# Optimization experiments

Hardware: AMD Instinct MI355X
Metric: run time of the kernel (lower is better)

Reference implementation:

```python
import jax, jax.numpy as jnp
import numpy as np

N, E, B = 50000, 640000, 4
H, L = 128, 4
NODE_IN, EDGE_IN, COND_IN, NODE_OUT = 12, 4, 10, 3


def _mlp(x, w1, b1, w2, b2):
    # Linear -> ReLU -> Linear
    return jnp.maximum(x @ w1 + b1, 0.0) @ w2 + b2


def setup_inputs() -> dict:
    key = jax.random.key(0)
    keys = iter(jax.random.split(key, 64))

    def p(*shape):
        fan_in = shape[-2] if len(shape) >= 2 else shape[-1]
        return (jax.random.normal(next(keys), shape, jnp.float32) / np.sqrt(fan_in)).astype(jnp.float32)

    inp = {
        "x": jax.random.normal(next(keys), (N, NODE_IN), jnp.float32),
        "edge_index": jax.random.randint(next(keys), (2, E), 0, N),
        "edge_attr": jax.random.normal(next(keys), (E, EDGE_IN), jnp.float32),
        "conditions": jax.random.normal(next(keys), (B, COND_IN), jnp.float32),
        "batch": jnp.sort(jax.random.randint(next(keys), (N,), 0, B)),
        # encoders
        "enc_node_w1": p(NODE_IN, H), "enc_node_b1": jnp.zeros((H,), jnp.float32),
        "enc_node_w2": p(H, H), "enc_node_b2": jnp.zeros((H,), jnp.float32),
        "enc_edge_w1": p(EDGE_IN, H), "enc_edge_b1": jnp.zeros((H,), jnp.float32),
        "enc_edge_w2": p(H, H), "enc_edge_b2": jnp.zeros((H,), jnp.float32),
        "enc_cond_w1": p(COND_IN, H), "enc_cond_b1": jnp.zeros((H,), jnp.float32),
        "enc_cond_w2": p(H, H), "enc_cond_b2": jnp.zeros((H,), jnp.float32),
        # shared MultiheadAttention: with a single key, softmax weight == 1 per head,
        # so output = out_proj(v_proj(kv)); q/k projections cancel exactly (and have
        # identically zero gradient), so only v/out projections are materialized.
        "attn_wv": p(H, H), "attn_bv": jnp.zeros((H,), jnp.float32),
        "attn_wo": p(H, H), "attn_bo": jnp.zeros((H,), jnp.float32),
        # processor layers (stacked over L)
        "pe_w1": p(L, 4 * H, H), "pe_b1": jnp.zeros((L, H), jnp.float32),
        "pe_w2": p(L, H, H), "pe_b2": jnp.zeros((L, H), jnp.float32),
        "pn_w1": p(L, 3 * H, H), "pn_b1": jnp.zeros((L, H), jnp.float32),
        "pn_w2": p(L, H, H), "pn_b2": jnp.zeros((L, H), jnp.float32),
        # decoder
        "dec_w1": p(H, H), "dec_b1": jnp.zeros((H,), jnp.float32),
        "dec_w2": p(H, NODE_OUT), "dec_b2": jnp.zeros((NODE_OUT,), jnp.float32),
    }
    return inp


def reference(x, edge_index, edge_attr, conditions, batch,
              enc_node_w1, enc_node_b1, enc_node_w2, enc_node_b2,
              enc_edge_w1, enc_edge_b1, enc_edge_w2, enc_edge_b2,
              enc_cond_w1, enc_cond_b1, enc_cond_w2, enc_cond_b2,
              attn_wv, attn_bv, attn_wo, attn_bo,
              pe_w1, pe_b1, pe_w2, pe_b2,
              pn_w1, pn_b1, pn_w2, pn_b2,
              dec_w1, dec_b1, dec_w2, dec_b2):
    n = x.shape[0]
    h = _mlp(x, enc_node_w1, enc_node_b1, enc_node_w2, enc_node_b2)           # [N,H]
    e = _mlp(edge_attr, enc_edge_w1, enc_edge_b1, enc_edge_w2, enc_edge_b2)   # [E,H]
    u = _mlp(conditions, enc_cond_w1, enc_cond_b1, enc_cond_w2, enc_cond_b2)  # [B,H]

    row, col = edge_index[0], edge_index[1]
    u_nodes = u[batch]                                                        # [N,H]
    # single-key cross-attention -> softmax over 1 key == 1 -> out_proj(v_proj(u))
    x_cond = (u_nodes @ attn_wv + attn_bv) @ attn_wo + attn_bo               # [N,H], same every layer
    u_edges = u_nodes[row]                                                    # u[batch[row]]

    for l in range(pe_w1.shape[0]):
        # edge update: cat([src, dest, edge_attr, u[batch_e]]) -> MLP
        e = _mlp(jnp.concatenate([h[row], h[col], e, u_edges], axis=1),
                 pe_w1[l], pe_b1[l], pe_w2[l], pe_b2[l])
        # scatter-add aggregation (index_add on row)
        agg = jax.ops.segment_sum(e, row, num_segments=n)                     # [N,H]
        # node update with residual
        h = h + _mlp(jnp.concatenate([h, agg, x_cond], axis=1),
                     pn_w1[l], pn_b1[l], pn_w2[l], pn_b2[l])

    return _mlp(h, dec_w1, dec_b1, dec_w2, dec_b2)                            # [N,node_out]
```

## Files before the change

kernel.cpp:

```cpp
#include <hip/hip_runtime.h>
#include <cstddef>

#define NN 50000
#define NNP 50048
#define NE 640000
#define NB 4
#define H  128
#define NL 4
#define TE 64
#define TEE 128

typedef unsigned int u32;
typedef unsigned short u16;
typedef __attribute__((ext_vector_type(8))) short bf16x8;
typedef __attribute__((ext_vector_type(4))) float f32x4;

__device__ __forceinline__ float bf2f(u16 s) {
    union { u32 u; float f; } v; v.u = ((u32)s) << 16; return v.f;
}
__device__ __forceinline__ u16 f2bf(float f) {
    union { float f; u32 u; } v; v.f = f;
    u32 u = v.u;
    u += 0x7FFF + ((u >> 16) & 1);
    return (u16)(u >> 16);
}
__device__ __forceinline__ void unpack8(uint4 raw, float* d) {
    d[0] = bf2f(raw.x & 0xFFFF); d[1] = bf2f(raw.x >> 16);
    d[2] = bf2f(raw.y & 0xFFFF); d[3] = bf2f(raw.y >> 16);
    d[4] = bf2f(raw.z & 0xFFFF); d[5] = bf2f(raw.z >> 16);
    d[6] = bf2f(raw.w & 0xFFFF); d[7] = bf2f(raw.w >> 16);
}
__device__ __forceinline__ uint4 pack8(const float* s) {
    uint4 pk;
    pk.x = (u32)f2bf(s[0]) | ((u32)f2bf(s[1]) << 16);
    pk.y = (u32)f2bf(s[2]) | ((u32)f2bf(s[3]) << 16);
    pk.z = (u32)f2bf(s[4]) | ((u32)f2bf(s[5]) << 16);
    pk.w = (u32)f2bf(s[6]) | ((u32)f2bf(s[7]) << 16);
    return pk;
}
__device__ __forceinline__ bf16x8 ld_f32_bf8(const float* __restrict__ p) {
    const float4 a = *(const float4*)p;
    const float4 b = *(const float4*)(p + 4);
    bf16x8 r;
    r[0] = (short)f2bf(a.x); r[1] = (short)f2bf(a.y);
    r[2] = (short)f2bf(a.z); r[3] = (short)f2bf(a.w);
    r[4] = (short)f2bf(b.x); r[5] = (short)f2bf(b.y);
    r[6] = (short)f2bf(b.z); r[7] = (short)f2bf(b.w);
    return r;
}

__global__ __launch_bounds__(256) void k_zero(float* __restrict__ p, int n4) {
    const int i = blockIdx.x * 256 + threadIdx.x;
    if (i < n4) ((float4*)p)[i] = make_float4(0.f, 0.f, 0.f, 0.f);
}

__global__ __launch_bounds__(256) void k_hist(const int* __restrict__ rowi,
                                              u32* __restrict__ cnt) {
    const int i = blockIdx.x * 256 + threadIdx.x;
    if (i < NE) atomicAdd(&cnt[rowi[i]], 1u);
}

__global__ __launch_bounds__(1024) void k_scan(u32* __restrict__ cnt) {
    __shared__ u32 part[1024];
    const int t = threadIdx.x;
    const int CHUNK = (NN + 1023) / 1024;
    const int lo = t * CHUNK;
    const int hi = (lo + CHUNK < NN) ? lo + CHUNK : NN;
    u32 s = 0;
    for (int i = lo; i < hi; ++i) s += cnt[i];
    part[t] = s;
    __syncthreads();
    for (int ofs = 1; ofs < 1024; ofs <<= 1) {
        const u32 v = (t >= ofs) ? part[t - ofs] : 0u;
        __syncthreads();
        part[t] += v;
        __syncthreads();
    }
    u32 run = (t == 0) ? 0u : part[t - 1];
    for (int i = lo; i < hi; ++i) { const u32 c = cnt[i]; cnt[i] = run; run += c; }
}

__global__ __launch_bounds__(256) void k_scatter(const int* __restrict__ rowi,
                                                 const int* __restrict__ coli,
                                                 u32* __restrict__ off,
                                                 int* __restrict__ permS,
                                                 int* __restrict__ rowS,
                                                 int* __restrict__ colS) {
    const int i = blockIdx.x * 256 + threadIdx.x;
    if (i < NE) {
        const int r = rowi[i];
        const u32 p = atomicAdd(&off[r], 1u);
        permS[p] = i; rowS[p] = r; colS[p] = coli[i];
    }
}

__global__ __launch_bounds__(256) void k_prep(
    const float* __restrict__ pe_w1, const float* __restrict__ pe_w2,
    const float* __restrict__ pn_w1, const float* __restrict__ pn_w2,
    const float* __restrict__ ew2,   const float* __restrict__ nw2,
    const float* __restrict__ dw1,
    u16* __restrict__ W1t, u16* __restrict__ W2t,
    u16* __restrict__ WaT, u16* __restrict__ WbT,
    u16* __restrict__ Wn1aT, u16* __restrict__ Wn1bT, u16* __restrict__ Wn2T,
    u16* __restrict__ W2et, u16* __restrict__ W2nt, u16* __restrict__ W1dt) {
    const int li = blockIdx.x;
    const float* src; u16* dst;
    switch (blockIdx.y) {
        case 0: src = pe_w1 + ((size_t)li * 512 + 256) * H; dst = W1t  + (size_t)li * H * H; break;
        case 1: src = pe_w2 + (size_t)li * H * H;           dst = W2t  + (size_t)li * H * H; break;
        case 2: src = pe_w1 + (size_t)li * 512 * H;         dst = WaT  + (size_t)li * H * H; break;
        case 3: src = pe_w1 + ((size_t)li * 512 + 128) * H; dst = WbT  + (size_t)li * H * H; break;
        case 4: src = pn_w1 + (size_t)li * 384 * H;         dst = Wn1aT + (size_t)li * H * H; break;
        case 5: src = pn_w1 + ((size_t)li * 384 + 128) * H; dst = Wn1bT + (size_t)li * H * H; break;
        case 6: src = pn_w2 + (size_t)li * H * H;           dst = Wn2T + (size_t)li * H * H; break;
        default:
            if (li == 0)      { src = ew2; dst = W2et; }
            else if (li == 1) { src = nw2; dst = W2nt; }
            else if (li == 2) { src = dw1; dst = W1dt; }
            else return;
            break;
    }
    for (int idx = threadIdx.x; idx < H * H; idx += 256) {
        const int n = idx >> 7, k = idx & 127;
        dst[idx] = f2bf(src[(size_t)k * H + n]);
    }
}

__global__ __launch_bounds__(128) void k_small(
    const float* __restrict__ cond,
    const float* __restrict__ ecw1, const float* __restrict__ ecb1,
    const float* __restrict__ ecw2, const float* __restrict__ ecb2,
    const float* __restrict__ wv, const float* __restrict__ bv,
    const float* __restrict__ wo, const float* __restrict__ bo,
    const float* __restrict__ pe_w1, const float* __restrict__ pe_b1,
    const float* __restrict__ pn_w1, const float* __restrict__ pn_b1,
    float* __restrict__ cbat, float* __restrict__ nbat) {
    __shared__ float tmp[NB][H];
    __shared__ float uL[NB][H];
    __shared__ float xcL[NB][H];
    const int t = threadIdx.x;
    for (int b = 0; b < NB; ++b) {
        float a = ecb1[t];
        for (int k = 0; k < 10; ++k) a = fmaf(cond[b * 10 + k], ecw1[k * H + t], a);
        tmp[b][t] = fmaxf(a, 0.f);
    }
    __syncthreads();
    for (int b = 0; b < NB; ++b) {
        float a = ecb2[t];
        for (int k = 0; k < H; ++k) a = fmaf(tmp[b][k], ecw2[k * H + t], a);
        uL[b][t] = a;
    }
    __syncthreads();
    for (int b = 0; b < NB; ++b) {
        float a = bv[t];
        for (int k = 0; k < H; ++k) a = fmaf(uL[b][k], wv[k * H + t], a);
        tmp[b][t] = a;
    }
    __syncthreads();
    for (int b = 0; b < NB; ++b) {
        float a = bo[t];
        for (int k = 0; k < H; ++k) a = fmaf(tmp[b][k], wo[k * H + t], a);
        xcL[b][t] = a;
    }
    __syncthreads();
    for (int l = 0; l < NL; ++l) {
        const float* w1u = pe_w1 + ((size_t)l * 512 + 384) * H;
        for (int b = 0; b < NB; ++b) {
            float a = pe_b1[l * H + t];
            for (int k = 0; k < H; ++k) a = fmaf(uL[b][k], w1u[k * H + t], a);
            cbat[(l * NB + b) * H + t] = a;
        }
        const float* w1x = pn_w1 + ((size_t)l * 384 + 256) * H;
        for (int b = 0; b < NB; ++b) {
            float a = pn_b1[l * H + t];
            for (int k = 0; k < H; ++k) a = fmaf(xcL[b][k], w1x[k * H + t], a);
            nbat[(l * NB + b) * H + t] = a;
        }
    }
}

__global__ __launch_bounds__(256) void k_enc_e_mfma(
    const float* __restrict__ ea,
    const int* __restrict__ permS,
    const float* __restrict__ w1, const float* __restrict__ b1,
    const u16* __restrict__ W2et, const float* __restrict__ b2,
    u16* __restrict__ e) {
    __shared__ float SI[TE][H + 4];
    const int t = threadIdx.x;
    const long long e0 = (long long)blockIdx.x * TE;
    const int w = t >> 6, l = t & 63;
    const int m16 = l & 15, g = l >> 4;
    const int row = w * 16 + m16;

    const int src = permS[e0 + row];
    const float4 av = *(const float4*)&ea[(size_t)src * 4];

    bf16x8 afrag[4];
#pragma unroll
    for (int ks = 0; ks < 4; ++ks) {
        const int c0 = ks * 32 + g * 8;
        float hv[8];
        {
            const float4 ba = *(const float4*)&b1[c0];
            const float4 bb = *(const float4*)&b1[c0 + 4];
            hv[0] = ba.x; hv[1] = ba.y; hv[2] = ba.z; hv[3] = ba.w;
            hv[4] = bb.x; hv[5] = bb.y; hv[6] = bb.z; hv[7] = bb.w;
        }
#pragma unroll
        for (int k = 0; k < 4; ++k) {
            const float s = (k == 0) ? av.x : (k == 1) ? av.y : (k == 2) ? av.z : av.w;
            const float4 wa = *(const float4*)&w1[k * H + c0];
            const float4 wb = *(const float4*)&w1[k * H + c0 + 4];
            hv[0] = fmaf(s, wa.x, hv[0]); hv[1] = fmaf(s, wa.y, hv[1]);
            hv[2] = fmaf(s, wa.z, hv[2]); hv[3] = fmaf(s, wa.w, hv[3]);
            hv[4] = fmaf(s, wb.x, hv[4]); hv[5] = fmaf(s, wb.y, hv[5]);
            hv[6] = fmaf(s, wb.z, hv[6]); hv[7] = fmaf(s, wb.w, hv[7]);
        }
#pragma unroll
        for (int j = 0; j < 8; ++j) afrag[ks][j] = (short)f2bf(fmaxf(hv[j], 0.f));
    }

    f32x4 acc[8];
#pragma unroll
    for (int nt = 0; nt < 8; ++nt) {
        const float bb = b2[nt * 16 + m16];
        acc[nt][0] = bb; acc[nt][1] = bb; acc[nt][2] = bb; acc[nt][3] = bb;
    }
#pragma unroll
    for (int ks = 0; ks < 4; ++ks) {
#pragma unroll
        for (int nt = 0; nt < 8; ++nt) {
            const bf16x8 bfr =
                *(const bf16x8*)&W2et[(size_t)(nt * 16 + m16) * H + ks * 32 + g * 8];
            acc[nt] = __builtin_amdgcn_mfma_f32_16x16x32_bf16(afrag[ks], bfr, acc[nt], 0, 0, 0);
        }
    }

#pragma unroll
    for (int nt = 0; nt < 8; ++nt)
#pragma unroll
        for (int j = 0; j < 4; ++j)
            SI[w * 16 + g * 4 + j][nt * 16 + m16] = acc[nt][j];
    __syncthreads();
    for (int u = t; u < TE * 16; u += 256) {
        const int j = u >> 4, c8 = (u & 15) * 8;
        *(uint4*)&e[(size_t)(e0 + j) * H + c8] = pack8(&SI[j][c8]);
    }
}

__global__ __launch_bounds__(256) void k_enc_n_mfma(
    const float* __restrict__ x,
    const float* __restrict__ w1, const float* __restrict__ b1,
    const u16* __restrict__ W2nt, const float* __restrict__ b2,
    float* __restrict__ h) {
    __shared__ float SI[TE][H + 4];
    const int t = threadIdx.x;
    const long long n0 = (long long)blockIdx.x * TE;
    const int w = t >> 6, l = t & 63;
    const int m16 = l & 15, g = l >> 4;
    const int row = w * 16 + m16;
    const long long nr = (n0 + row < NN) ? (n0 + row) : (NN - 1);

    float av[12];
    {
        const float4 a0 = *(const float4*)&x[nr * 12];
        const float4 a1 = *(const float4*)&x[nr * 12 + 4];
        const float4 a2 = *(const float4*)&x[nr * 12 + 8];
        av[0] = a0.x; av[1] = a0.y; av[2] = a0.z; av[3] = a0.w;
        av[4] = a1.x; av[5] = a1.y; av[6] = a1.z; av[7] = a1.w;
        av[8] = a2.x; av[9] = a2.y; av[10] = a2.z; av[11] = a2.w;
    }

    bf16x8 afrag[4];
#pragma unroll
    for (int ks = 0; ks < 4; ++ks) {
        const int c0 = ks * 32 + g * 8;
        float hv[8];
        {
            const float4 ba = *(const float4*)&b1[c0];
            const float4 bb = *(const float4*)&b1[c0 + 4];
            hv[0] = ba.x; hv[1] = ba.y; hv[2] = ba.z; hv[3] = ba.w;
            hv[4] = bb.x; hv[5] = bb.y; hv[6] = bb.z; hv[7] = bb.w;
        }
#pragma unroll
        for (int k = 0; k < 12; ++k) {
            const float s = av[k];
            const float4 wa = *(const float4*)&w1[k * H + c0];
            const float4 wb = *(const float4*)&w1[k * H + c0 + 4];
            hv[0] = fmaf(s, wa.x, hv[0]); hv[1] = fmaf(s, wa.y, hv[1]);
            hv[2] = fmaf(s, wa.z, hv[2]); hv[3] = fmaf(s, wa.w, hv[3]);
            hv[4] = fmaf(s, wb.x, hv[4]); hv[5] = fmaf(s, wb.y, hv[5]);
            hv[6] = fmaf(s, wb.z, hv[6]); hv[7] = fmaf(s, wb.w, hv[7]);
        }
#pragma unroll
        for (int j = 0; j < 8; ++j) afrag[ks][j] = (short)f2bf(fmaxf(hv[j], 0.f));
    }

    f32x4 acc[8];
#pragma unroll
    for (int nt = 0; nt < 8; ++nt) {
        const float bb = b2[nt * 16 + m16];
        acc[nt][0] = bb; acc[nt][1] = bb; acc[nt][2] = bb; acc[nt][3] = bb;
    }
#pragma unroll
    for (int ks = 0; ks < 4; ++ks) {
#pragma unroll
        for (int nt = 0; nt < 8; ++nt) {
            const bf16x8 bfr =
                *(const bf16x8*)&W2nt[(size_t)(nt * 16 + m16) * H + ks * 32 + g * 8];
            acc[nt] = __builtin_amdgcn_mfma_f32_16x16x32_bf16(afrag[ks], bfr, acc[nt], 0, 0, 0);
        }
    }

#pragma unroll
    for (int nt = 0; nt < 8; ++nt)
#pragma unroll
        for (int j = 0; j < 4; ++j)
            SI[w * 16 + g * 4 + j][nt * 16 + m16] = acc[nt][j];
    __syncthreads();
    for (int u = t; u < TE * H / 4; u += 256) {
        const int j = u >> 5, c4 = (u & 31) * 4;
        *(float4*)&h[(size_t)(n0 + j) * H + c4] = *(const float4*)&SI[j][c4];
    }
}

__global__ __launch_bounds__(256) void k_gemm_dual_mfma(
    const float* __restrict__ h,
    const u16* __restrict__ WaT, const u16* __restrict__ WbT,
    const float* __restrict__ cbatl, const int* __restrict__ batch,
    u16* __restrict__ Ca, u16* __restrict__ Cb) {
    __shared__ u16 SI[TE][H + 8];
    __shared__ float CB[NB][H];
    __shared__ int bL[TE];
    const int t = threadIdx.x;
    const long long n0 = (long long)blockIdx.x * TE;
    const int w = t >> 6, l = t & 63;
    const int m16 = l & 15, g = l >> 4;
    const int row = w * 16 + m16;

    if (t < TE) {
        const long long n = n0 + t;
        bL[t] = batch[n < NN ? n : (NN - 1)];
    }
    for (int i = t; i < NB * H; i += 256) ((float*)CB)[i] = cbatl[i];

    bf16x8 afrag[4];
    {
        const float* hp = h + (size_t)(n0 + row) * H + g * 8;
#pragma unroll
        for (int ks = 0; ks < 4; ++ks) afrag[ks] = ld_f32_bf8(hp + ks * 32);
    }
    __syncthreads();

    f32x4 accA[8], accB[8];
#pragma unroll
    for (int nt = 0; nt < 8; ++nt) {
#pragma unroll
        for (int j = 0; j < 4; ++j)
            accA[nt][j] = CB[bL[w * 16 + g * 4 + j]][nt * 16 + m16];
        accB[nt][0] = 0.f; accB[nt][1] = 0.f; accB[nt][2] = 0.f; accB[nt][3] = 0.f;
    }
#pragma unroll
    for (int ks = 0; ks < 4; ++ks) {
#pragma unroll
        for (int nt = 0; nt < 8; ++nt) {
            const size_t off = (size_t)(nt * 16 + m16) * H + ks * 32 + g * 8;
            const bf16x8 ba = *(const bf16x8*)&WaT[off];
            const bf16x8 bb = *(const bf16x8*)&WbT[off];
            accA[nt] = __builtin_amdgcn_mfma_f32_16x16x32_bf16(afrag[ks], ba, accA[nt], 0, 0, 0);
            accB[nt] = __builtin_amdgcn_mfma_f32_16x16x32_bf16(afrag[ks], bb, accB[nt], 0, 0, 0);
        }
    }

#pragma unroll
    for (int s = 0; s < 2; ++s) {
        __syncthreads();
#pragma unroll
        for (int nt = 0; nt < 8; ++nt)
#pragma unroll
            for (int j = 0; j < 4; ++j)
                SI[w * 16 + g * 4 + j][nt * 16 + m16] =
                    f2bf(s ? accB[nt][j] : accA[nt][j]);
        __syncthreads();
        u16* C = s ? Cb : Ca;
        for (int u = t; u < TE * 16; u += 256) {
            const int j = u >> 4, c8 = (u & 15) * 8;
            *(uint4*)&C[(size_t)(n0 + j) * H + c8] = *(const uint4*)&SI[j][c8];
        }
    }
}

template <bool WRITE_E>
__global__ __launch_bounds__(256, 2) void k_edge_mfma(
    const u16* __restrict__ hA, const u16* __restrict__ hB,
    const u16* __restrict__ W1t, const u16* __restrict__ W2t,
    const float* __restrict__ b2,
    const int* __restrict__ rowS, const int* __restrict__ colS,
    u16* __restrict__ e, float* __restrict__ agg) {
    __shared__ u16 SI[TEE][H + 8];
    const int t = threadIdx.x;
    const long long e0 = (long long)blockIdx.x * TEE;
    const int w = t >> 6, l = t & 63;
    const int m16 = l & 15, g = l >> 4;

    bf16x8 af0[4], af1[4];
    {
        const u16* ep0 = e + (size_t)(e0 + w * 32 + m16) * H + g * 8;
        const u16* ep1 = ep0 + 16 * H;
#pragma unroll
        for (int ks = 0; ks < 4; ++ks) {
            af0[ks] = *(const bf16x8*)(ep0 + ks * 32);
            af1[ks] = *(const bf16x8*)(ep1 + ks * 32);
        }
    }

    {
        int rj[8], cj[8];
#pragma unroll
        for (int it = 0; it < 8; ++it) {
            const int j = (l + it * 64) >> 4;
            rj[it] = rowS[e0 + w * 32 + j];
            cj[it] = colS[e0 + w * 32 + j];
        }
#pragma unroll
        for (int it = 0; it < 8; ++it) {
            const int u = l + it * 64;
            const int j = u >> 4, c8 = (u & 15) * 8;
            float va[8], vb[8], sm[8];
            unpack8(*(const uint4*)&hA[(size_t)rj[it] * H + c8], va);
            unpack8(*(const uint4*)&hB[(size_t)cj[it] * H + c8], vb);
#pragma unroll
            for (int q = 0; q < 8; ++q) sm[q] = va[q] + vb[q];
            *(uint4*)&SI[w * 32 + j][c8] = pack8(sm);
        }
    }

    f32x4 acc0[8], acc1[8];
#pragma unroll
    for (int nt = 0; nt < 8; ++nt) {
#pragma unroll
        for (int j = 0; j < 4; ++j) {
            acc0[nt][j] = bf2f(SI[w * 32 + g * 4 + j][nt * 16 + m16]);
            acc1[nt][j] = bf2f(SI[w * 32 + 16 + g * 4 + j][nt * 16 + m16]);
        }
    }
#pragma unroll
    for (int ks = 0; ks < 4; ++ks) {
#pragma unroll
        for (int nt = 0; nt < 8; ++nt) {
            const bf16x8 bfr =
                *(const bf16x8*)&W1t[(size_t)(nt * 16 + m16) * H + ks * 32 + g * 8];
            acc0[nt] = __builtin_amdgcn_mfma_f32_16x16x32_bf16(af0[ks], bfr, acc0[nt], 0, 0, 0);
            acc1[nt] = __builtin_amdgcn_mfma_f32_16x16x32_bf16(af1[ks], bfr, acc1[nt], 0, 0, 0);
        }
    }

#pragma unroll
    for (int nt = 0; nt < 8; ++nt)
#pragma unroll
        for (int j = 0; j < 4; ++j) {
            SI[w * 32 + g * 4 + j][nt * 16 + m16]      = f2bf(fmaxf(acc0[nt][j], 0.f));
            SI[w * 32 + 16 + g * 4 + j][nt * 16 + m16] = f2bf(fmaxf(acc1[nt][j], 0.f));
        }

#pragma unroll
    for (int nt = 0; nt < 8; ++nt) {
        const float bb = b2[nt * 16 + m16];
        acc0[nt][0] = bb; acc0[nt][1] = bb; acc0[nt][2] = bb; acc0[nt][3] = bb;
        acc1[nt][0] = bb; acc1[nt][1] = bb; acc1[nt][2] = bb; acc1[nt][3] = bb;
    }
#pragma unroll
    for (int ks = 0; ks < 4; ++ks) {
        const bf16x8 a20 = *(const bf16x8*)&SI[w * 32 + m16][ks * 32 + g * 8];
        const bf16x8 a21 = *(const bf16x8*)&SI[w * 32 + 16 + m16][ks * 32 + g * 8];
#pragma unroll
        for (int nt = 0; nt < 8; ++nt) {
            const bf16x8 bfr =
                *(const bf16x8*)&W2t[(size_t)(nt * 16 + m16) * H + ks * 32 + g * 8];
            acc0[nt] = __builtin_amdgcn_mfma_f32_16x16x32_bf16(a20, bfr, acc0[nt], 0, 0, 0);
            acc1[nt] = __builtin_amdgcn_mfma_f32_16x16x32_bf16(a21, bfr, acc1[nt], 0, 0, 0);
        }
    }

    {
        int r[8];
#pragma unroll
        for (int j = 0; j < 4; ++j) {
            r[j]     = rowS[e0 + w * 32 + g * 4 + j];
            r[4 + j] = rowS[e0 + w * 32 + 16 + g * 4 + j];
        }
#pragma unroll
        for (int nt = 0; nt < 8; ++nt) {
            const int c = nt * 16 + m16;
            float v[8];
#pragma unroll
            for (int j = 0; j < 4; ++j) { v[j] = acc0[nt][j]; v[4 + j] = acc1[nt][j]; }
            float s = v[0];
            int prev = r[0];
#pragma unroll
            for (int j = 1; j < 8; ++j) {
                if (r[j] == prev) s += v[j];
                else { atomicAdd(&agg[(size_t)prev * H + c], s); s = v[j]; prev = r[j]; }
            }
            atomicAdd(&agg[(size_t)prev * H + c], s);
        }
    }

    if (WRITE_E) {
#pragma unroll
        for (int nt = 0; nt < 8; ++nt)
#pragma unroll
            for (int j = 0; j < 4; ++j) {
                SI[w * 32 + g * 4 + j][nt * 16 + m16]      = f2bf(acc0[nt][j]);
                SI[w * 32 + 16 + g * 4 + j][nt * 16 + m16] = f2bf(acc1[nt][j]);
            }
#pragma unroll
        for (int it = 0; it < 8; ++it) {
            const int u = l + it * 64;
            const int j = u >> 4, c8 = (u & 15) * 8;
            *(uint4*)&e[(size_t)(e0 + w * 32 + j) * H + c8] = *(const uint4*)&SI[w * 32 + j][c8];
        }
    }
}

__global__ __launch_bounds__(256) void k_node_mfma(
    const u16* __restrict__ Wn1aT, const u16* __restrict__ Wn1bT,
    const u16* __restrict__ Wn2T, const float* __restrict__ bn2,
    const float* __restrict__ nbatl, const int* __restrict__ batch,
    const float* __restrict__ agg, float* __restrict__ h) {
    __shared__ float SI[TE][H + 4];
    __shared__ float NBl[NB][H];
    __shared__ int bL[TE];
    const int t = threadIdx.x;
    const long long n0 = (long long)blockIdx.x * TE;
    if (t < TE) {
        const long long n = n0 + t;
        bL[t] = batch[n < NN ? n : (NN - 1)];
    }
    for (int i = t; i < NB * H; i += 256) ((float*)NBl)[i] = nbatl[i];

    const int w = t >> 6, l = t & 63;
    const int m16 = l & 15, g = l >> 4;
    const int row = w * 16 + m16;

    bf16x8 afrag[4];
    {
        const float* hp = h + (size_t)(n0 + row) * H + g * 8;
#pragma unroll
        for (int ks = 0; ks < 4; ++ks) afrag[ks] = ld_f32_bf8(hp + ks * 32);
    }
    __syncthreads();

    f32x4 acc[8];
#pragma unroll
    for (int nt = 0; nt < 8; ++nt)
#pragma unroll
        for (int j = 0; j < 4; ++j)
            acc[nt][j] = NBl[bL[w * 16 + g * 4 + j]][nt * 16 + m16];

#pragma unroll
    for (int ks = 0; ks < 4; ++ks)
#pragma unroll
        for (int nt = 0; nt < 8; ++nt) {
            const bf16x8 bfr =
                *(const bf16x8*)&Wn1aT[(size_t)(nt * 16 + m16) * H + ks * 32 + g * 8];
            acc[nt] = __builtin_amdgcn_mfma_f32_16x16x32_bf16(afrag[ks], bfr, acc[nt], 0, 0, 0);
        }

    {
        const float* ap = agg + (size_t)(n0 + row) * H + g * 8;
#pragma unroll
        for (int ks = 0; ks < 4; ++ks) afrag[ks] = ld_f32_bf8(ap + ks * 32);
    }
#pragma unroll
    for (int ks = 0; ks < 4; ++ks)
#pragma unroll
        for (int nt = 0; nt < 8; ++nt) {
            const bf16x8 bfr =
                *(const bf16x8*)&Wn1bT[(size_t)(nt * 16 + m16) * H + ks * 32 + g * 8];
            acc[nt] = __builtin_amdgcn_mfma_f32_16x16x32_bf16(afrag[ks], bfr, acc[nt], 0, 0, 0);
        }

#pragma unroll
    for (int nt = 0; nt < 8; ++nt)
#pragma unroll
        for (int j = 0; j < 4; ++j)
            SI[w * 16 + g * 4 + j][nt * 16 + m16] = fmaxf(acc[nt][j], 0.f);
    __syncthreads();

    f32x4 acc2[8];
#pragma unroll
    for (int nt = 0; nt < 8; ++nt) {
        const float bb = bn2[nt * 16 + m16];
        acc2[nt][0] = bb; acc2[nt][1] = bb; acc2[nt][2] = bb; acc2[nt][3] = bb;
    }
#pragma unroll
    for (int ks = 0; ks < 4; ++ks) {
        bf16x8 a2;
        const float* hp = &SI[w * 16 + m16][ks * 32 + g * 8];
#pragma unroll
        for (int j = 0; j < 8; ++j) a2[j] = (short)f2bf(hp[j]);
#pragma unroll
        for (int nt = 0; nt < 8; ++nt) {
            const bf16x8 bfr =
                *(const bf16x8*)&Wn2T[(size_t)(nt * 16 + m16) * H + ks * 32 + g * 8];
            acc2[nt] = __builtin_amdgcn_mfma_f32_16x16x32_bf16(a2, bfr, acc2[nt], 0, 0, 0);
        }
    }
    __syncthreads();

#pragma unroll
    for (int nt = 0; nt < 8; ++nt)
#pragma unroll
        for (int j = 0; j < 4; ++j)
            SI[w * 16 + g * 4 + j][nt * 16 + m16] = acc2[nt][j];
    __syncthreads();

    for (int u = t; u < TE * H / 4; u += 256) {
        const int j = u >> 5, c4 = (u & 31) * 4;
        float4 hv = *(const float4*)&h[(size_t)(n0 + j) * H + c4];
        const float4 sv = *(const float4*)&SI[j][c4];
        hv.x += sv.x; hv.y += sv.y; hv.z += sv.z; hv.w += sv.w;
        *(float4*)&h[(size_t)(n0 + j) * H + c4] = hv;
    }
}

__global__ __launch_bounds__(256) void k_dec_mfma(
    const float* __restrict__ h,
    const u16* __restrict__ W1dt, const float* __restrict__ b1,
    const float* __restrict__ w2, const float* __restrict__ b2,
    float* __restrict__ out) {
    __shared__ float SI[TE][H + 4];
    const int t = threadIdx.x;
    const long long n0 = (long long)blockIdx.x * TE;
    const int w = t >> 6, l = t & 63;
    const int m16 = l & 15, g = l >> 4;
    const int row = w * 16 + m16;

    bf16x8 afrag[4];
    {
        const float* hp = h + (size_t)(n0 + row) * H + g * 8;
#pragma unroll
        for (int ks = 0; ks < 4; ++ks) afrag[ks] = ld_f32_bf8(hp + ks * 32);
    }

    f32x4 acc[8];
#pragma unroll
    for (int nt = 0; nt < 8; ++nt) {
        const float bb = b1[nt * 16 + m16];
        acc[nt][0] = bb; acc[nt][1] = bb; acc[nt][2] = bb; acc[nt][3] = bb;
    }
#pragma unroll
    for (int ks = 0; ks < 4; ++ks) {
#pragma unroll
        for (int nt = 0; nt < 8; ++nt) {
            const bf16x8 bfr =
                *(const bf16x8*)&W1dt[(size_t)(nt * 16 + m16) * H + ks * 32 + g * 8];
            acc[nt] = __builtin_amdgcn_mfma_f32_16x16x32_bf16(afrag[ks], bfr, acc[nt], 0, 0, 0);
        }
    }

#pragma unroll
    for (int nt = 0; nt < 8; ++nt)
#pragma unroll
        for (int j = 0; j < 4; ++j)
            SI[w * 16 + g * 4 + j][nt * 16 + m16] = fmaxf(acc[nt][j], 0.f);
    __syncthreads();

    if (t < TE * 3) {
        const int n = t / 3, c = t - n * 3;
        if (n0 + n < NN) {
            float v = b2[c];
            for (int k = 0; k < H; ++k) v = fmaf(SI[n][k], w2[k * 3 + c], v);
            out[(size_t)(n0 + n) * 3 + c] = v;
        }
    }
}

extern "C" void kernel_launch(void* const* d_in, const int* in_sizes, int n_in,
                              void* d_out, int out_size, void* d_ws, size_t ws_size,
                              hipStream_t stream) {
    const float* x          = (const float*)d_in[0];
    const int*   edge_index = (const int*)d_in[1];
    const float* edge_attr  = (const float*)d_in[2];
    const float* cond       = (const float*)d_in[3];
    const int*   batch      = (const int*)d_in[4];
    const float* enc_node_w1 = (const float*)d_in[5];
    const float* enc_node_b1 = (const float*)d_in[6];
    const float* enc_node_w2 = (const float*)d_in[7];
    const float* enc_node_b2 = (const float*)d_in[8];
    const float* enc_edge_w1 = (const float*)d_in[9];
    const float* enc_edge_b1 = (const float*)d_in[10];
    const float* enc_edge_w2 = (const float*)d_in[11];
    const float* enc_edge_b2 = (const float*)d_in[12];
    const float* enc_cond_w1 = (const float*)d_in[13];
    const float* enc_cond_b1 = (const float*)d_in[14];
    const float* enc_cond_w2 = (const float*)d_in[15];
    const float* enc_cond_b2 = (const float*)d_in[16];
    const float* attn_wv = (const float*)d_in[17];
    const float* attn_bv = (const float*)d_in[18];
    const float* attn_wo = (const float*)d_in[19];
    const float* attn_bo = (const float*)d_in[20];
    const float* pe_w1 = (const float*)d_in[21];
    const float* pe_b1 = (const float*)d_in[22];
    const float* pe_w2 = (const float*)d_in[23];
    const float* pe_b2 = (const float*)d_in[24];
    const float* pn_w1 = (const float*)d_in[25];
    const float* pn_b1 = (const float*)d_in[26];
    const float* pn_w2 = (const float*)d_in[27];
    const float* pn_b2 = (const float*)d_in[28];
    const float* dec_w1 = (const float*)d_in[29];
    const float* dec_b1 = (const float*)d_in[30];
    const float* dec_w2 = (const float*)d_in[31];
    const float* dec_b2 = (const float*)d_in[32];

    u16*   e    = (u16*)d_ws;
    float* h    = (float*)((char*)d_ws + (size_t)NE * H * 2);
    float* agg  = h + (size_t)NNP * H;
    u16*   hA   = (u16*)(agg + (size_t)NNP * H);
    u16*   hB   = hA + (size_t)NNP * H;
    float* cbat = (float*)(hB + (size_t)NNP * H);
    float* nbat = cbat + NL * NB * H;
    u16*   W1t   = (u16*)(nbat + NL * NB * H);
    u16*   W2t   = W1t  + (size_t)NL * H * H;
    u16*   WaT   = W2t  + (size_t)NL * H * H;
    u16*   WbT   = WaT  + (size_t)NL * H * H;
    u16*   Wn1aT = WbT  + (size_t)NL * H * H;
    u16*   Wn1bT = Wn1aT + (size_t)NL * H * H;
    u16*   Wn2T  = Wn1bT + (size_t)NL * H * H;
    u16*   W2et  = Wn2T + (size_t)NL * H * H;
    u16*   W2nt  = W2et + (size_t)H * H;
    u16*   W1dt  = W2nt + (size_t)H * H;
    u32*   cnt   = (u32*)(W1dt + (size_t)H * H);
    int*   permS = (int*)(cnt + NNP);
    int*   rowS  = permS + NE;
    int*   colS  = rowS + NE;

    const int* rowi = edge_index;
    const int* coli = edge_index + NE;
    float* out = (float*)d_out;

    k_zero<<<(NNP / 4 + 255) / 256, 256, 0, stream>>>((float*)cnt, NNP / 4);
    k_hist<<<NE / 256, 256, 0, stream>>>(rowi, cnt);
    k_scan<<<1, 1024, 0, stream>>>(cnt);
    k_scatter<<<NE / 256, 256, 0, stream>>>(rowi, coli, cnt, permS, rowS, colS);

    k_prep<<<dim3(NL, 8), 256, 0, stream>>>(pe_w1, pe_w2, pn_w1, pn_w2,
                                            enc_edge_w2, enc_node_w2, dec_w1,
                                            W1t, W2t, WaT, WbT,
                                            Wn1aT, Wn1bT, Wn2T, W2et, W2nt, W1dt);
    k_small<<<1, 128, 0, stream>>>(cond, enc_cond_w1, enc_cond_b1, enc_cond_w2, enc_cond_b2,
                                   attn_wv, attn_bv, attn_wo, attn_bo,
                                   pe_w1, pe_b1, pn_w1, pn_b1, cbat, nbat);
    k_enc_n_mfma<<<NNP / TE, 256, 0, stream>>>(
        x, enc_node_w1, enc_node_b1, W2nt, enc_node_b2, h);
    k_enc_e_mfma<<<NE / TE, 256, 0, stream>>>(
        edge_attr, permS, enc_edge_w1, enc_edge_b1, W2et, enc_edge_b2, e);

    for (int l = 0; l < NL; ++l) {
        k_zero<<<(NNP * H / 4 + 255) / 256, 256, 0, stream>>>(agg, NNP * H / 4);
        k_gemm_dual_mfma<<<NNP / TE, 256, 0, stream>>>(
            h, WaT + (size_t)l * H * H, WbT + (size_t)l * H * H,
            cbat + l * NB * H, batch, hA, hB);
        if (l < NL - 1)
            k_edge_mfma<true><<<NE / TEE, 256, 0, stream>>>(
                hA, hB, W1t + (size_t)l * H * H, W2t + (size_t)l * H * H,
                pe_b2 + l * H, rowS, colS, e, agg);
        else
            k_edge_mfma<false><<<NE / TEE, 256, 0, stream>>>(
                hA, hB, W1t + (size_t)l * H * H, W2t + (size_t)l * H * H,
                pe_b2 + l * H, rowS, colS, e, agg);
        k_node_mfma<<<NNP / TE, 256, 0, stream>>>(
            Wn1aT + (size_t)l * H * H, Wn1bT + (size_t)l * H * H,
            Wn2T + (size_t)l * H * H, pn_b2 + l * H,
            nbat + l * NB * H, batch, agg, h);
    }
    k_dec_mfma<<<NNP / TE, 256, 0, stream>>>(h, W1dt, dec_b1, dec_w2, dec_b2, out);
}
```

Measured before the change: 2.363 ms.

## Fuse agg zeroing into dual GEMM, drop block syncs, swizzle edge block order

Zeroing of the aggregation buffer moves into the dual GEMM kernel, which removes a separate kernel launch and pass per layer. The node kernel and edge encoder now keep their shared-memory staging per wave, so block-wide barriers go away, and the node kernel reads batch bias directly from global memory instead of staging it in LDS. The edge kernel remaps block indices with an 8-way interleave, which changes the order edge tiles are processed and with it L2 locality and atomic contention. The risks are extra global loads in the node kernel and the untested effect of the block reordering on cache behaviour.

```diff
diff --git a/kernel.cpp b/kernel.cpp
--- a/kernel.cpp
+++ b/kernel.cpp
@@ -241,10 +241,11 @@
 #pragma unroll
         for (int j = 0; j < 4; ++j)
             SI[w * 16 + g * 4 + j][nt * 16 + m16] = acc[nt][j];
-    __syncthreads();
-    for (int u = t; u < TE * 16; u += 256) {
+#pragma unroll
+    for (int it = 0; it < 4; ++it) {
+        const int u = l + it * 64;
         const int j = u >> 4, c8 = (u & 15) * 8;
-        *(uint4*)&e[(size_t)(e0 + j) * H + c8] = pack8(&SI[j][c8]);
+        *(uint4*)&e[(size_t)(e0 + w * 16 + j) * H + c8] = pack8(&SI[w * 16 + j][c8]);
     }
 }
 
@@ -328,7 +329,7 @@
     const float* __restrict__ h,
     const u16* __restrict__ WaT, const u16* __restrict__ WbT,
     const float* __restrict__ cbatl, const int* __restrict__ batch,
-    u16* __restrict__ Ca, u16* __restrict__ Cb) {
+    u16* __restrict__ Ca, u16* __restrict__ Cb, float* __restrict__ agg) {
     __shared__ u16 SI[TE][H + 8];
     __shared__ float CB[NB][H];
     __shared__ int bL[TE];
@@ -337,6 +338,14 @@
     const int w = t >> 6, l = t & 63;
     const int m16 = l & 15, g = l >> 4;
     const int row = w * 16 + m16;
+
+    {
+        const float4 z4 = make_float4(0.f, 0.f, 0.f, 0.f);
+        for (int u = t; u < TE * H / 4; u += 256) {
+            const int j = u >> 5, c4 = (u & 31) * 4;
+            *(float4*)&agg[(size_t)(n0 + j) * H + c4] = z4;
+        }
+    }
 
     if (t < TE) {
         const long long n = n0 + t;
@@ -399,7 +408,8 @@
     u16* __restrict__ e, float* __restrict__ agg) {
     __shared__ u16 SI[TEE][H + 8];
     const int t = threadIdx.x;
-    const long long e0 = (long long)blockIdx.x * TEE;
+    const int bid = (blockIdx.x & 7) * ((int)gridDim.x >> 3) + (blockIdx.x >> 3);
+    const long long e0 = (long long)bid * TEE;
     const int w = t >> 6, l = t & 63;
     const int m16 = l & 15, g = l >> 4;
 
@@ -529,16 +539,8 @@
     const float* __restrict__ nbatl, const int* __restrict__ batch,
     const float* __restrict__ agg, float* __restrict__ h) {
     __shared__ float SI[TE][H + 4];
-    __shared__ float NBl[NB][H];
-    __shared__ int bL[TE];
     const int t = threadIdx.x;
     const long long n0 = (long long)blockIdx.x * TE;
-    if (t < TE) {
-        const long long n = n0 + t;
-        bL[t] = batch[n < NN ? n : (NN - 1)];
-    }
-    for (int i = t; i < NB * H; i += 256) ((float*)NBl)[i] = nbatl[i];
-
     const int w = t >> 6, l = t & 63;
     const int m16 = l & 15, g = l >> 4;
     const int row = w * 16 + m16;
@@ -549,14 +551,20 @@
 #pragma unroll
         for (int ks = 0; ks < 4; ++ks) afrag[ks] = ld_f32_bf8(hp + ks * 32);
     }
-    __syncthreads();
+
+    int bj[4];
+#pragma unroll
+    for (int j = 0; j < 4; ++j) {
+        const long long n = n0 + w * 16 + g * 4 + j;
+        bj[j] = batch[n < NN ? n : (NN - 1)];
+    }
 
     f32x4 acc[8];
 #pragma unroll
     for (int nt = 0; nt < 8; ++nt)
 #pragma unroll
         for (int j = 0; j < 4; ++j)
-            acc[nt][j] = NBl[bL[w * 16 + g * 4 + j]][nt * 16 + m16];
+            acc[nt][j] = nbatl[(size_t)bj[j] * H + nt * 16 + m16];
 
 #pragma unroll
     for (int ks = 0; ks < 4; ++ks)
@@ -586,13 +594,11 @@
 #pragma unroll
         for (int j = 0; j < 4; ++j)
             SI[w * 16 + g * 4 + j][nt * 16 + m16] = fmaxf(acc[nt][j], 0.f);
-    __syncthreads();
-
-    f32x4 acc2[8];
+
 #pragma unroll
     for (int nt = 0; nt < 8; ++nt) {
         const float bb = bn2[nt * 16 + m16];
-        acc2[nt][0] = bb; acc2[nt][1] = bb; acc2[nt][2] = bb; acc2[nt][3] = bb;
+        acc[nt][0] = bb; acc[nt][1] = bb; acc[nt][2] = bb; acc[nt][3] = bb;
     }
 #pragma unroll
     for (int ks = 0; ks < 4; ++ks) {
@@ -604,24 +610,24 @@
         for (int nt = 0; nt < 8; ++nt) {
             const bf16x8 bfr =
                 *(const bf16x8*)&Wn2T[(size_t)(nt * 16 + m16) * H + ks * 32 + g * 8];
-            acc2[nt] = __builtin_amdgcn_mfma_f32_16x16x32_bf16(a2, bfr, acc2[nt], 0, 0, 0);
-        }
-    }
-    __syncthreads();
+            acc[nt] = __builtin_amdgcn_mfma_f32_16x16x32_bf16(a2, bfr, acc[nt], 0, 0, 0);
+        }
+    }
 
 #pragma unroll
     for (int nt = 0; nt < 8; ++nt)
 #pragma unroll
         for (int j = 0; j < 4; ++j)
-            SI[w * 16 + g * 4 + j][nt * 16 + m16] = acc2[nt][j];
-    __syncthreads();
-
-    for (int u = t; u < TE * H / 4; u += 256) {
+            SI[w * 16 + g * 4 + j][nt * 16 + m16] = acc[nt][j];
+
+#pragma unroll
+    for (int it = 0; it < 8; ++it) {
+        const int u = l + it * 64;
         const int j = u >> 5, c4 = (u & 31) * 4;
-        float4 hv = *(const float4*)&h[(size_t)(n0 + j) * H + c4];
-        const float4 sv = *(const float4*)&SI[j][c4];
+        float4 hv = *(const float4*)&h[(size_t)(n0 + w * 16 + j) * H + c4];
+        const float4 sv = *(const float4*)&SI[w * 16 + j][c4];
         hv.x += sv.x; hv.y += sv.y; hv.z += sv.z; hv.w += sv.w;
-        *(float4*)&h[(size_t)(n0 + j) * H + c4] = hv;
+        *(float4*)&h[(size_t)(n0 + w * 16 + j) * H + c4] = hv;
     }
 }
 
@@ -758,10 +764,9 @@
         edge_attr, permS, enc_edge_w1, enc_edge_b1, W2et, enc_edge_b2, e);
 
     for (int l = 0; l < NL; ++l) {
-        k_zero<<<(NNP * H / 4 + 255) / 256, 256, 0, stream>>>(agg, NNP * H / 4);
         k_gemm_dual_mfma<<<NNP / TE, 256, 0, stream>>>(
             h, WaT + (size_t)l * H * H, WbT + (size_t)l * H * H,
-            cbat + l * NB * H, batch, hA, hB);
+            cbat + l * NB * H, batch, hA, hB, agg);
         if (l < NL - 1)
             k_edge_mfma<true><<<NE / TEE, 256, 0, stream>>>(
                 hA, hB, W1t + (size_t)l * H * H, W2t + (size_t)l * H * H,
```

New measurement: 2.319 ms. About the same (-1.9%).
